# Optimization experiments

Hardware: AMD Instinct MI355X
Metric: run time of the kernel (lower is better)

Reference implementation:

```python
import jax, jax.numpy as jnp
import numpy as np

NUM_FEATURES = 256
NUM_PIDS = 5554          # must equal hardcoded FocalLoss ignore_index
NUM_CQ = 50000
N_ROIS = 2048
OIM_SCALAR = 30.0
IGNORE_INDEX = 5554
ALPHA = 1.0
GAMMA = 2.0


def _l2norm(x):
    return x / jnp.linalg.norm(x, axis=-1, keepdims=True)


def setup_inputs() -> dict:
    key = jax.random.key(0)
    k1, k2, k3, k4, k5 = jax.random.split(key, 5)
    inputs = _l2norm(jax.random.normal(k1, (N_ROIS, NUM_FEATURES), jnp.float32))
    # targets >= 1 so label = targets-1 >= 0 (the inds filter is all-True -> static shapes)
    # targets == NUM_PIDS+1 -> label == NUM_PIDS == ignore_index (unlabeled, ignored in loss)
    targets = jax.random.randint(k2, (N_ROIS,), 1, NUM_PIDS + 2, dtype=jnp.int64)
    ious = jax.random.uniform(k3, (N_ROIS,), jnp.float32)
    lut = _l2norm(jax.random.normal(k4, (NUM_PIDS, NUM_FEATURES), jnp.float32))
    cq = _l2norm(jax.random.normal(k5, (NUM_CQ, NUM_FEATURES), jnp.float32))
    return {"inputs": inputs, "lut": lut, "cq": cq, "targets": targets, "ious": ious}


def _focal_loss(logits, labels):
    # F.cross_entropy(reduction='none', ignore_index=IGNORE_INDEX) then
    # focal = alpha * (1-pt)^gamma * ce, mean over ALL samples (ignored -> 0).
    logp = jax.nn.log_softmax(logits, axis=-1)                       # [N, C]
    ce = -jnp.take_along_axis(logp, labels[:, None], axis=1)[:, 0]   # [N]
    ce = jnp.where(labels == IGNORE_INDEX, 0.0, ce)
    pt = jnp.exp(-ce)
    return jnp.mean(ALPHA * (1.0 - pt) ** GAMMA * ce)


def reference(inputs, lut, cq, targets, ious):
    # targets = cat(roi_label); label = targets - 1; inds all True by construction.
    label = targets - 1
    # LOIM forward: logits against labeled LUT and unlabeled circular queue.
    table = jnp.concatenate([lut, cq], axis=0)          # [P+Q, D]
    projected = OIM_SCALAR * (inputs @ table.T)         # [N, P+Q]
    loss_oim = _focal_loss(projected, label)
    return loss_oim, inputs, label
```

## Files before the change

### kernel.cpp

```cpp
#include <hip/hip_runtime.h>
#include <hip/hip_bf16.h>


#define NFEAT 256
#define NROIS 2048
#define NPIDS 5554
#define NCLS 55554
#define NCHUNKS 3473
#define S2F 43.280851226668906f
#define LN2F 0.6931471805599453f
#define LOFF 524289

typedef float f32x4 __attribute__((ext_vector_type(4)));
typedef short bf16x8 __attribute__((ext_vector_type(8)));

#if __has_builtin(__builtin_amdgcn_exp2f)
#define EXP2(x) __builtin_amdgcn_exp2f(x)
#else
#define EXP2(x) exp2f(x)
#endif

__device__ __forceinline__ short bfb(float x) {
    return __builtin_bit_cast(short, __float2bfloat16(x));
}

__global__ __launch_bounds__(256) void prep(const int* __restrict__ cand0,
                                            const int* __restrict__ cand1,
                                            int* __restrict__ lab,
                                            float* __restrict__ S) {
    __shared__ int smode;
    __shared__ const int* sT;
    if (threadIdx.x == 0) {
        const int* T = cand0;
        const unsigned u0 = (unsigned)cand0[0];
        const float f0 = __builtin_bit_cast(float, cand0[0]);
        const bool oki = (u0 >= 1u && u0 <= 6000u);
        const bool okf = (f0 >= 1.0f && f0 <= 6000.0f);
        if (!oki && !okf) T = cand1;
        int mode = 0;
        const unsigned tu0 = (unsigned)T[0];
        const float tf0 = __builtin_bit_cast(float, T[0]);
        if (tu0 >= 1u && tu0 <= 6000u) mode = ((T[1] | T[3] | T[5] | T[7]) == 0) ? 1 : 0;
        else if (tf0 >= 1.0f && tf0 <= 6000.0f) mode = 2;
        smode = mode; sT = T;
    }
    __syncthreads();
    const int mode = smode;
    const int* T = sT;
    for (int j = threadIdx.x; j < NROIS; j += 256) {
        int tv;
        if (mode == 1)      tv = T[2 * j];
        else if (mode == 2) tv = (int)__builtin_bit_cast(float, T[j]);
        else                tv = T[j];
        lab[j] = tv - 1;
    }
    for (int j = threadIdx.x; j < NROIS + 1; j += 256) S[j] = 0.0f;
}

__global__ __launch_bounds__(256) void cvt_table(const float* __restrict__ lut,
                                                 const float* __restrict__ cq,
                                                 unsigned short* __restrict__ tb) {
    const size_t LUTN = (size_t)NPIDS * NFEAT;
    const size_t TOT  = (size_t)NCLS * NFEAT;
    size_t i = ((size_t)blockIdx.x * 256 + threadIdx.x) * 4;
    const size_t stride = (size_t)gridDim.x * 256 * 4;
    for (; i < TOT; i += stride) {
        float4 v;
        if (i < LUTN) v = *reinterpret_cast<const float4*>(lut + i);
        else          v = *reinterpret_cast<const float4*>(cq + (i - LUTN));
        ushort4 o;
        o.x = (unsigned short)bfb(v.x); o.y = (unsigned short)bfb(v.y);
        o.z = (unsigned short)bfb(v.z); o.w = (unsigned short)bfb(v.w);
        *reinterpret_cast<ushort4*>(tb + i) = o;
    }
}

__global__ __launch_bounds__(256) void writeout(const float* __restrict__ inputs,
                                                const int* __restrict__ lab,
                                                float* __restrict__ f) {
    const int i = blockIdx.x * 256 + threadIdx.x;
    const float4 v = *reinterpret_cast<const float4*>(inputs + (size_t)i * 4);
    float* o = f + 1 + (size_t)i * 4;
    o[0] = v.x; o[1] = v.y; o[2] = v.z; o[3] = v.w;
    if (i < NROIS) f[LOFF + i] = __bfloat162float(__float2bfloat16((float)lab[i]));
}

template <bool TB>
__global__ __launch_bounds__(256, 2) void main_gemm2(const float* __restrict__ inputs,
                                                     const unsigned short* __restrict__ tb,
                                                     const float* __restrict__ lut,
                                                     const float* __restrict__ cq,
                                                     float* __restrict__ S) {
    __shared__ short ldsb[2][4096];
    const int tid = threadIdx.x;
    const int lane = tid & 63;
    const int wave = tid >> 6;
    const int cs = blockIdx.x & 63;
    const int rg = blockIdx.x >> 6;
    const int rowbase = rg * 256 + wave * 64;
    const int li = lane & 15;
    const int q = lane >> 4;
    const int xorli = 4 * (li & 7);

    bf16x8 afrag[4][8];
    #pragma unroll
    for (int s = 0; s < 4; s++) {
        const float* rp = inputs + (size_t)(rowbase + s * 16 + li) * NFEAT + q * 8;
        #pragma unroll
        for (int kc = 0; kc < 8; kc++) {
            const float4 x0 = *reinterpret_cast<const float4*>(rp + kc * 32);
            const float4 x1 = *reinterpret_cast<const float4*>(rp + kc * 32 + 4);
            bf16x8 a;
            a[0] = bfb(x0.x); a[1] = bfb(x0.y); a[2] = bfb(x0.z); a[3] = bfb(x0.w);
            a[4] = bfb(x1.x); a[5] = bfb(x1.y); a[6] = bfb(x1.z); a[7] = bfb(x1.w);
            afrag[s][kc] = a;
        }
    }

    const int s0 = tid, s1 = tid + 256;
    const int cc0 = s0 >> 5, cc1 = s1 >> 5;
    const int uo0 = ((s0 & 31) ^ (4 * (cc0 & 7))) * 8;
    const int uo1 = ((s1 & 31) ^ (4 * (cc1 & 7))) * 8;

    const int cA = (cs * NCHUNKS) >> 6;
    const int cB = ((cs + 1) * NCHUNKS) >> 6;

    float sums[4][4] = {{0.f,0.f,0.f,0.f},{0.f,0.f,0.f,0.f},
                        {0.f,0.f,0.f,0.f},{0.f,0.f,0.f,0.f}};

    {
        int n0 = cA * 16 + cc0; n0 = n0 < (NCLS - 1) ? n0 : (NCLS - 1);
        int n1 = cA * 16 + cc1; n1 = n1 < (NCLS - 1) ? n1 : (NCLS - 1);
        if (TB) {
            const bf16x8 v0 = *reinterpret_cast<const bf16x8*>(tb + (size_t)n0 * NFEAT + uo0);
            const bf16x8 v1 = *reinterpret_cast<const bf16x8*>(tb + (size_t)n1 * NFEAT + uo1);
            *reinterpret_cast<bf16x8*>(&ldsb[0][s0 * 8]) = v0;
            *reinterpret_cast<bf16x8*>(&ldsb[0][s1 * 8]) = v1;
        } else {
            const float* r0 = ((n0 < NPIDS) ? lut + (size_t)n0 * NFEAT
                                            : cq + (size_t)(n0 - NPIDS) * NFEAT) + uo0;
            const float* r1 = ((n1 < NPIDS) ? lut + (size_t)n1 * NFEAT
                                            : cq + (size_t)(n1 - NPIDS) * NFEAT) + uo1;
            const float4 a0 = *reinterpret_cast<const float4*>(r0);
            const float4 a1 = *reinterpret_cast<const float4*>(r0 + 4);
            const float4 b0 = *reinterpret_cast<const float4*>(r1);
            const float4 b1 = *reinterpret_cast<const float4*>(r1 + 4);
            bf16x8 v0, v1;
            v0[0]=bfb(a0.x); v0[1]=bfb(a0.y); v0[2]=bfb(a0.z); v0[3]=bfb(a0.w);
            v0[4]=bfb(a1.x); v0[5]=bfb(a1.y); v0[6]=bfb(a1.z); v0[7]=bfb(a1.w);
            v1[0]=bfb(b0.x); v1[1]=bfb(b0.y); v1[2]=bfb(b0.z); v1[3]=bfb(b0.w);
            v1[4]=bfb(b1.x); v1[5]=bfb(b1.y); v1[6]=bfb(b1.z); v1[7]=bfb(b1.w);
            *reinterpret_cast<bf16x8*>(&ldsb[0][s0 * 8]) = v0;
            *reinterpret_cast<bf16x8*>(&ldsb[0][s1 * 8]) = v1;
        }
    }
    __syncthreads();

    int cur = 0;
    for (int ci = cA; ci < cB; ++ci) {
        const bool pf = (ci + 1 < cB);
        bf16x8 p0, p1;
        float4 f0a, f0b, f1a, f1b;
        if (pf) {
            int n0 = (ci + 1) * 16 + cc0; n0 = n0 < (NCLS - 1) ? n0 : (NCLS - 1);
            int n1 = (ci + 1) * 16 + cc1; n1 = n1 < (NCLS - 1) ? n1 : (NCLS - 1);
            if (TB) {
                p0 = *reinterpret_cast<const bf16x8*>(tb + (size_t)n0 * NFEAT + uo0);
                p1 = *reinterpret_cast<const bf16x8*>(tb + (size_t)n1 * NFEAT + uo1);
            } else {
                const float* r0 = ((n0 < NPIDS) ? lut + (size_t)n0 * NFEAT
                                                : cq + (size_t)(n0 - NPIDS) * NFEAT) + uo0;
                const float* r1 = ((n1 < NPIDS) ? lut + (size_t)n1 * NFEAT
                                                : cq + (size_t)(n1 - NPIDS) * NFEAT) + uo1;
                f0a = *reinterpret_cast<const float4*>(r0);
                f0b = *reinterpret_cast<const float4*>(r0 + 4);
                f1a = *reinterpret_cast<const float4*>(r1);
                f1b = *reinterpret_cast<const float4*>(r1 + 4);
            }
        }
        f32x4 acc[4] = {{0.f,0.f,0.f,0.f},{0.f,0.f,0.f,0.f},
                        {0.f,0.f,0.f,0.f},{0.f,0.f,0.f,0.f}};
        #pragma unroll
        for (int kc = 0; kc < 8; kc++) {
            const int slot = li * 32 + ((q + 4 * kc) ^ xorli);
            const bf16x8 b = *reinterpret_cast<const bf16x8*>(&ldsb[cur][slot * 8]);
            acc[0] = __builtin_amdgcn_mfma_f32_16x16x32_bf16(afrag[0][kc], b, acc[0], 0, 0, 0);
            acc[1] = __builtin_amdgcn_mfma_f32_16x16x32_bf16(afrag[1][kc], b, acc[1], 0, 0, 0);
            acc[2] = __builtin_amdgcn_mfma_f32_16x16x32_bf16(afrag[2][kc], b, acc[2], 0, 0, 0);
            acc[3] = __builtin_amdgcn_mfma_f32_16x16x32_bf16(afrag[3][kc], b, acc[3], 0, 0, 0);
        }
        const float valid = ((ci * 16 + li) < NCLS) ? 1.0f : 0.0f;
        #pragma unroll
        for (int s = 0; s < 4; s++)
            #pragma unroll
            for (int r = 0; r < 4; r++)
                sums[s][r] += valid * EXP2(S2F * (acc[s][r] - 1.0f));
        if (pf) {
            if (!TB) {
                p0[0]=bfb(f0a.x); p0[1]=bfb(f0a.y); p0[2]=bfb(f0a.z); p0[3]=bfb(f0a.w);
                p0[4]=bfb(f0b.x); p0[5]=bfb(f0b.y); p0[6]=bfb(f0b.z); p0[7]=bfb(f0b.w);
                p1[0]=bfb(f1a.x); p1[1]=bfb(f1a.y); p1[2]=bfb(f1a.z); p1[3]=bfb(f1a.w);
                p1[4]=bfb(f1b.x); p1[5]=bfb(f1b.y); p1[6]=bfb(f1b.z); p1[7]=bfb(f1b.w);
            }
            *reinterpret_cast<bf16x8*>(&ldsb[cur ^ 1][s0 * 8]) = p0;
            *reinterpret_cast<bf16x8*>(&ldsb[cur ^ 1][s1 * 8]) = p1;
        }
        __syncthreads();
        cur ^= 1;
    }

    #pragma unroll
    for (int s = 0; s < 4; s++)
        #pragma unroll
        for (int r = 0; r < 4; r++) {
            float v = sums[s][r];
            v += __shfl_xor(v, 1); v += __shfl_xor(v, 2);
            v += __shfl_xor(v, 4); v += __shfl_xor(v, 8);
            sums[s][r] = v;
        }
    if (li == 0) {
        #pragma unroll
        for (int s = 0; s < 4; s++)
            #pragma unroll
            for (int r = 0; r < 4; r++)
                atomicAdd(&S[rowbase + s * 16 + q * 4 + r], sums[s][r]);
    }
}

__global__ __launch_bounds__(256) void focal_final(const float* __restrict__ inputs,
                                                   const float* __restrict__ lut,
                                                   const int* __restrict__ lab,
                                                   const float* __restrict__ S,
                                                   float* __restrict__ loss_acc) {
    const int wave = threadIdx.x >> 6;
    const int lane = threadIdx.x & 63;
    const int row = blockIdx.x * 4 + wave;
    const int label = lab[row];
    const bool valid = (label >= 0 && label < NPIDS);
    const int lr = valid ? label : 0;
    const float4 a = *reinterpret_cast<const float4*>(inputs + (size_t)row * NFEAT + lane * 4);
    const float4 b = *reinterpret_cast<const float4*>(lut + (size_t)lr * NFEAT + lane * 4);
    float v = a.x * b.x + a.y * b.y + a.z * b.z + a.w * b.w;
    #pragma unroll
    for (int m = 1; m < 64; m <<= 1) v += __shfl_xor(v, m);

    __shared__ float red[4];
    if (lane == 0) {
        float fo = 0.0f;
        if (valid) {
            const float l2 = v * S2F;
            const float lse2 = S2F + log2f(S[row]);
            float ce = fmaxf((lse2 - l2) * LN2F, 0.0f);
            const float pt = EXP2(l2 - lse2);
            const float om = 1.0f - pt;
            fo = om * om * ce;
        }
        red[wave] = fo;
    }
    __syncthreads();
    if (threadIdx.x == 0) atomicAdd(loss_acc, red[0] + red[1] + red[2] + red[3]);
}

__global__ void loss_write(const float* __restrict__ loss_acc, float* __restrict__ f) {
    if (threadIdx.x == 0 && blockIdx.x == 0) f[0] = loss_acc[0] * (1.0f / NROIS);
}

extern "C" void kernel_launch(void* const* d_in, const int* in_sizes, int n_in,
                              void* d_out, int out_size, void* d_ws, size_t ws_size,
                              hipStream_t stream) {
    const float* inputs = (const float*)d_in[0];
    const float* lut    = (const float*)d_in[1];
    const float* cq     = (const float*)d_in[2];
    const int*   cand0  = (const int*)d_in[3];
    const int*   cand1  = (const int*)((n_in > 4) ? d_in[4] : d_in[3]);
    float* f = (float*)d_out;

    const size_t TBB = (size_t)NCLS * NFEAT * 2;
    char* ws = (char*)d_ws;
    const bool useTB = ws_size >= TBB + 32768;

    unsigned short* tb = useTB ? (unsigned short*)ws : nullptr;
    float* S        = useTB ? (float*)(ws + TBB) : (float*)ws;
    float* loss_acc = S + NROIS;
    int*   lab      = (int*)(S + NROIS + 1);

    prep<<<1, 256, 0, stream>>>(cand0, cand1, lab, S);
    if (useTB) cvt_table<<<4096, 256, 0, stream>>>(lut, cq, tb);
    writeout<<<512, 256, 0, stream>>>(inputs, lab, f);
    if (useTB) main_gemm2<true><<<512, 256, 0, stream>>>(inputs, tb, lut, cq, S);
    else       main_gemm2<false><<<512, 256, 0, stream>>>(inputs, tb, lut, cq, S);
    focal_final<<<512, 256, 0, stream>>>(inputs, lut, lab, S, loss_acc);
    loss_write<<<1, 64, 0, stream>>>(loss_acc, f);
}
```

Baseline: 193.0 us.

## Fuse preprocessing kernels, triple-buffer GEMM with direct global-to-LDS loads

Merges prep, table conversion and writeout into one preprocessing kernel that also pre-converts inputs to bf16 and pads the table with zero rows. The GEMM's fast path now streams table tiles straight into LDS with global_load_lds into a three-stage ring guarded by manual waitcnt/barrier, which removes register staging and the per-chunk validity mask. The final loss write is folded into focal_final through a last-block counter. Together these cut kernel launches and load latency, at the cost of extra workspace and reliance on hand-written waitcnt ordering. Padded rows still add exp(-S2F) terms, which is only a tiny approximation.

Result: faster. 176.7 us (-8.5%).

```diff
diff --git a/kernel.cpp b/kernel.cpp
--- a/kernel.cpp
+++ b/kernel.cpp
@@ -7,12 +7,14 @@
 #define NPIDS 5554
 #define NCLS 55554
 #define NCHUNKS 3473
+#define NCLSP (NCHUNKS * 16)
 #define S2F 43.280851226668906f
 #define LN2F 0.6931471805599453f
 #define LOFF 524289
 
 typedef float f32x4 __attribute__((ext_vector_type(4)));
 typedef short bf16x8 __attribute__((ext_vector_type(8)));
+typedef unsigned short u16x8 __attribute__((ext_vector_type(8)));
 
 #if __has_builtin(__builtin_amdgcn_exp2f)
 #define EXP2(x) __builtin_amdgcn_exp2f(x)
@@ -24,74 +26,95 @@
     return __builtin_bit_cast(short, __float2bfloat16(x));
 }
 
-__global__ __launch_bounds__(256) void prep(const int* __restrict__ cand0,
-                                            const int* __restrict__ cand1,
-                                            int* __restrict__ lab,
-                                            float* __restrict__ S) {
-    __shared__ int smode;
-    __shared__ const int* sT;
-    if (threadIdx.x == 0) {
-        const int* T = cand0;
-        const unsigned u0 = (unsigned)cand0[0];
-        const float f0 = __builtin_bit_cast(float, cand0[0]);
-        const bool oki = (u0 >= 1u && u0 <= 6000u);
-        const bool okf = (f0 >= 1.0f && f0 <= 6000.0f);
-        if (!oki && !okf) T = cand1;
-        int mode = 0;
-        const unsigned tu0 = (unsigned)T[0];
-        const float tf0 = __builtin_bit_cast(float, T[0]);
-        if (tu0 >= 1u && tu0 <= 6000u) mode = ((T[1] | T[3] | T[5] | T[7]) == 0) ? 1 : 0;
-        else if (tf0 >= 1.0f && tf0 <= 6000.0f) mode = 2;
-        smode = mode; sT = T;
-    }
-    __syncthreads();
-    const int mode = smode;
-    const int* T = sT;
-    for (int j = threadIdx.x; j < NROIS; j += 256) {
-        int tv;
-        if (mode == 1)      tv = T[2 * j];
-        else if (mode == 2) tv = (int)__builtin_bit_cast(float, T[j]);
-        else                tv = T[j];
-        lab[j] = tv - 1;
-    }
-    for (int j = threadIdx.x; j < NROIS + 1; j += 256) S[j] = 0.0f;
-}
-
-__global__ __launch_bounds__(256) void cvt_table(const float* __restrict__ lut,
-                                                 const float* __restrict__ cq,
-                                                 unsigned short* __restrict__ tb) {
-    const size_t LUTN = (size_t)NPIDS * NFEAT;
-    const size_t TOT  = (size_t)NCLS * NFEAT;
-    size_t i = ((size_t)blockIdx.x * 256 + threadIdx.x) * 4;
-    const size_t stride = (size_t)gridDim.x * 256 * 4;
-    for (; i < TOT; i += stride) {
-        float4 v;
-        if (i < LUTN) v = *reinterpret_cast<const float4*>(lut + i);
-        else          v = *reinterpret_cast<const float4*>(cq + (i - LUTN));
-        ushort4 o;
-        o.x = (unsigned short)bfb(v.x); o.y = (unsigned short)bfb(v.y);
-        o.z = (unsigned short)bfb(v.z); o.w = (unsigned short)bfb(v.w);
-        *reinterpret_cast<ushort4*>(tb + i) = o;
-    }
-}
-
-__global__ __launch_bounds__(256) void writeout(const float* __restrict__ inputs,
-                                                const int* __restrict__ lab,
-                                                float* __restrict__ f) {
-    const int i = blockIdx.x * 256 + threadIdx.x;
-    const float4 v = *reinterpret_cast<const float4*>(inputs + (size_t)i * 4);
-    float* o = f + 1 + (size_t)i * 4;
-    o[0] = v.x; o[1] = v.y; o[2] = v.z; o[3] = v.w;
-    if (i < NROIS) f[LOFF + i] = __bfloat162float(__float2bfloat16((float)lab[i]));
+__device__ __forceinline__ void gll16(const void* g, void* l) {
+    __builtin_amdgcn_global_load_lds(
+        (const __attribute__((address_space(1))) void*)g,
+        (__attribute__((address_space(3))) void*)l, 16, 0, 0);
+}
+
+__global__ __launch_bounds__(256) void preprocess(
+        const float* __restrict__ inputs, const float* __restrict__ lut,
+        const float* __restrict__ cq, const int* __restrict__ cand0,
+        const int* __restrict__ cand1, unsigned short* __restrict__ tb,
+        unsigned short* __restrict__ ab, int* __restrict__ lab,
+        float* __restrict__ S, float* __restrict__ f, const int useTB) {
+    const int tid = threadIdx.x;
+    const int bx = blockIdx.x;
+
+    if (bx == 0) {
+        __shared__ int smode;
+        __shared__ const int* sT;
+        if (tid == 0) {
+            const int* T = cand0;
+            const unsigned u0 = (unsigned)cand0[0];
+            const float f0 = __builtin_bit_cast(float, cand0[0]);
+            const bool oki = (u0 >= 1u && u0 <= 6000u);
+            const bool okf = (f0 >= 1.0f && f0 <= 6000.0f);
+            if (!oki && !okf) T = cand1;
+            int mode = 0;
+            const unsigned tu0 = (unsigned)T[0];
+            const float tf0 = __builtin_bit_cast(float, T[0]);
+            if (tu0 >= 1u && tu0 <= 6000u) mode = ((T[1] | T[3] | T[5] | T[7]) == 0) ? 1 : 0;
+            else if (tf0 >= 1.0f && tf0 <= 6000.0f) mode = 2;
+            smode = mode; sT = T;
+        }
+        __syncthreads();
+        const int mode = smode;
+        const int* T = sT;
+        for (int j = tid; j < NROIS; j += 256) {
+            int tv;
+            if (mode == 1)      tv = T[2 * j];
+            else if (mode == 2) tv = (int)__builtin_bit_cast(float, T[j]);
+            else                tv = T[j];
+            const int lv = tv - 1;
+            lab[j] = lv;
+            f[LOFF + j] = __bfloat162float(__float2bfloat16((float)lv));
+        }
+        for (int j = tid; j < NROIS + 8; j += 256) S[j] = 0.0f;
+    }
+
+    if (bx < 512) {
+        const int i = bx * 256 + tid;
+        const float4 v = *reinterpret_cast<const float4*>(inputs + (size_t)i * 4);
+        float* o = f + 1 + (size_t)i * 4;
+        o[0] = v.x; o[1] = v.y; o[2] = v.z; o[3] = v.w;
+        if (useTB) {
+            ushort4 u;
+            u.x = (unsigned short)bfb(v.x); u.y = (unsigned short)bfb(v.y);
+            u.z = (unsigned short)bfb(v.z); u.w = (unsigned short)bfb(v.w);
+            *reinterpret_cast<ushort4*>(ab + (size_t)i * 4) = u;
+        }
+    }
+
+    if (useTB) {
+        const size_t LUTN = (size_t)NPIDS * NFEAT;
+        const size_t TOT  = (size_t)NCLS * NFEAT;
+        const size_t TOTP = (size_t)NCLSP * NFEAT;
+        const size_t stride = (size_t)gridDim.x * 256 * 8;
+        for (size_t e = ((size_t)bx * 256 + tid) * 8; e < TOTP; e += stride) {
+            u16x8 o = {0, 0, 0, 0, 0, 0, 0, 0};
+            if (e < TOT) {
+                const float* sp = (e < LUTN) ? (lut + e) : (cq + (e - LUTN));
+                const float4 a = *reinterpret_cast<const float4*>(sp);
+                const float4 b = *reinterpret_cast<const float4*>(sp + 4);
+                o[0] = (unsigned short)bfb(a.x); o[1] = (unsigned short)bfb(a.y);
+                o[2] = (unsigned short)bfb(a.z); o[3] = (unsigned short)bfb(a.w);
+                o[4] = (unsigned short)bfb(b.x); o[5] = (unsigned short)bfb(b.y);
+                o[6] = (unsigned short)bfb(b.z); o[7] = (unsigned short)bfb(b.w);
+            }
+            *reinterpret_cast<u16x8*>(tb + e) = o;
+        }
+    }
 }
 
 template <bool TB>
-__global__ __launch_bounds__(256, 2) void main_gemm2(const float* __restrict__ inputs,
+__global__ __launch_bounds__(256, 2) void main_gemm3(const float* __restrict__ inputs,
                                                      const unsigned short* __restrict__ tb,
+                                                     const unsigned short* __restrict__ ab,
                                                      const float* __restrict__ lut,
                                                      const float* __restrict__ cq,
                                                      float* __restrict__ S) {
-    __shared__ short ldsb[2][4096];
+    __shared__ short ldsb[3][4096];
     const int tid = threadIdx.x;
     const int lane = tid & 63;
     const int wave = tid >> 6;
@@ -103,17 +126,27 @@
     const int xorli = 4 * (li & 7);
 
     bf16x8 afrag[4][8];
-    #pragma unroll
-    for (int s = 0; s < 4; s++) {
-        const float* rp = inputs + (size_t)(rowbase + s * 16 + li) * NFEAT + q * 8;
+    if constexpr (TB) {
         #pragma unroll
-        for (int kc = 0; kc < 8; kc++) {
-            const float4 x0 = *reinterpret_cast<const float4*>(rp + kc * 32);
-            const float4 x1 = *reinterpret_cast<const float4*>(rp + kc * 32 + 4);
-            bf16x8 a;
-            a[0] = bfb(x0.x); a[1] = bfb(x0.y); a[2] = bfb(x0.z); a[3] = bfb(x0.w);
-            a[4] = bfb(x1.x); a[5] = bfb(x1.y); a[6] = bfb(x1.z); a[7] = bfb(x1.w);
-            afrag[s][kc] = a;
+        for (int s = 0; s < 4; s++) {
+            const unsigned short* rp = ab + (size_t)(rowbase + s * 16 + li) * NFEAT + q * 8;
+            #pragma unroll
+            for (int kc = 0; kc < 8; kc++)
+                afrag[s][kc] = *reinterpret_cast<const bf16x8*>(rp + kc * 32);
+        }
+    } else {
+        #pragma unroll
+        for (int s = 0; s < 4; s++) {
+            const float* rp = inputs + (size_t)(rowbase + s * 16 + li) * NFEAT + q * 8;
+            #pragma unroll
+            for (int kc = 0; kc < 8; kc++) {
+                const float4 x0 = *reinterpret_cast<const float4*>(rp + kc * 32);
+                const float4 x1 = *reinterpret_cast<const float4*>(rp + kc * 32 + 4);
+                bf16x8 a;
+                a[0] = bfb(x0.x); a[1] = bfb(x0.y); a[2] = bfb(x0.z); a[3] = bfb(x0.w);
+                a[4] = bfb(x1.x); a[5] = bfb(x1.y); a[6] = bfb(x1.z); a[7] = bfb(x1.w);
+                afrag[s][kc] = a;
+            }
         }
     }
 
@@ -124,19 +157,58 @@
 
     const int cA = (cs * NCHUNKS) >> 6;
     const int cB = ((cs + 1) * NCHUNKS) >> 6;
+    const int NB = cB - cA;
 
     float sums[4][4] = {{0.f,0.f,0.f,0.f},{0.f,0.f,0.f,0.f},
                         {0.f,0.f,0.f,0.f},{0.f,0.f,0.f,0.f}};
-
-    {
-        int n0 = cA * 16 + cc0; n0 = n0 < (NCLS - 1) ? n0 : (NCLS - 1);
-        int n1 = cA * 16 + cc1; n1 = n1 < (NCLS - 1) ? n1 : (NCLS - 1);
-        if (TB) {
-            const bf16x8 v0 = *reinterpret_cast<const bf16x8*>(tb + (size_t)n0 * NFEAT + uo0);
-            const bf16x8 v1 = *reinterpret_cast<const bf16x8*>(tb + (size_t)n1 * NFEAT + uo1);
-            *reinterpret_cast<bf16x8*>(&ldsb[0][s0 * 8]) = v0;
-            *reinterpret_cast<bf16x8*>(&ldsb[0][s1 * 8]) = v1;
-        } else {
+    char* const lbase = (char*)&ldsb[0][0];
+
+    if constexpr (TB) {
+        const int ld0 = wave * 1024;
+        const int ld1 = 4096 + wave * 1024;
+        const unsigned short* p0 = tb + (size_t)(cA * 16 + cc0) * NFEAT + uo0;
+        const unsigned short* p1 = tb + (size_t)(cA * 16 + cc1) * NFEAT + uo1;
+        int ob0 = 0, ob1 = 8192, ob2 = 16384;
+
+        gll16(p0, lbase + ob0 + ld0);
+        gll16(p1, lbase + ob0 + ld1);
+        p0 += 16 * NFEAT; p1 += 16 * NFEAT;
+        if (NB > 1) {
+            gll16(p0, lbase + ob1 + ld0);
+            gll16(p1, lbase + ob1 + ld1);
+            p0 += 16 * NFEAT; p1 += 16 * NFEAT;
+        }
+
+        for (int i = 0; i < NB; ++i) {
+            if (i + 1 < NB) asm volatile("s_waitcnt vmcnt(2)\n\ts_barrier" ::: "memory");
+            else            asm volatile("s_waitcnt vmcnt(0)\n\ts_barrier" ::: "memory");
+            if (i + 2 < NB) {
+                gll16(p0, lbase + ob2 + ld0);
+                gll16(p1, lbase + ob2 + ld1);
+                p0 += 16 * NFEAT; p1 += 16 * NFEAT;
+            }
+            f32x4 acc[4] = {{0.f,0.f,0.f,0.f},{0.f,0.f,0.f,0.f},
+                            {0.f,0.f,0.f,0.f},{0.f,0.f,0.f,0.f}};
+            #pragma unroll
+            for (int kc = 0; kc < 8; kc++) {
+                const int slot = li * 32 + ((q + 4 * kc) ^ xorli);
+                const bf16x8 b = *reinterpret_cast<const bf16x8*>(lbase + ob0 + slot * 16);
+                acc[0] = __builtin_amdgcn_mfma_f32_16x16x32_bf16(afrag[0][kc], b, acc[0], 0, 0, 0);
+                acc[1] = __builtin_amdgcn_mfma_f32_16x16x32_bf16(afrag[1][kc], b, acc[1], 0, 0, 0);
+                acc[2] = __builtin_amdgcn_mfma_f32_16x16x32_bf16(afrag[2][kc], b, acc[2], 0, 0, 0);
+                acc[3] = __builtin_amdgcn_mfma_f32_16x16x32_bf16(afrag[3][kc], b, acc[3], 0, 0, 0);
+            }
+            #pragma unroll
+            for (int s = 0; s < 4; s++)
+                #pragma unroll
+                for (int r = 0; r < 4; r++)
+                    sums[s][r] += EXP2(S2F * acc[s][r] - S2F);
+            const int t = ob0; ob0 = ob1; ob1 = ob2; ob2 = t;
+        }
+    } else {
+        {
+            int n0 = cA * 16 + cc0; n0 = n0 < (NCLS - 1) ? n0 : (NCLS - 1);
+            int n1 = cA * 16 + cc1; n1 = n1 < (NCLS - 1) ? n1 : (NCLS - 1);
             const float* r0 = ((n0 < NPIDS) ? lut + (size_t)n0 * NFEAT
                                             : cq + (size_t)(n0 - NPIDS) * NFEAT) + uo0;
             const float* r1 = ((n1 < NPIDS) ? lut + (size_t)n1 * NFEAT
@@ -153,21 +225,14 @@
             *reinterpret_cast<bf16x8*>(&ldsb[0][s0 * 8]) = v0;
             *reinterpret_cast<bf16x8*>(&ldsb[0][s1 * 8]) = v1;
         }
-    }
-    __syncthreads();
-
-    int cur = 0;
-    for (int ci = cA; ci < cB; ++ci) {
-        const bool pf = (ci + 1 < cB);
-        bf16x8 p0, p1;
-        float4 f0a, f0b, f1a, f1b;
-        if (pf) {
-            int n0 = (ci + 1) * 16 + cc0; n0 = n0 < (NCLS - 1) ? n0 : (NCLS - 1);
-            int n1 = (ci + 1) * 16 + cc1; n1 = n1 < (NCLS - 1) ? n1 : (NCLS - 1);
-            if (TB) {
-                p0 = *reinterpret_cast<const bf16x8*>(tb + (size_t)n0 * NFEAT + uo0);
-                p1 = *reinterpret_cast<const bf16x8*>(tb + (size_t)n1 * NFEAT + uo1);
-            } else {
+        __syncthreads();
+        int cur = 0;
+        for (int ci = cA; ci < cB; ++ci) {
+            const bool pf = (ci + 1 < cB);
+            float4 f0a, f0b, f1a, f1b;
+            if (pf) {
+                int n0 = (ci + 1) * 16 + cc0; n0 = n0 < (NCLS - 1) ? n0 : (NCLS - 1);
+                int n1 = (ci + 1) * 16 + cc1; n1 = n1 < (NCLS - 1) ? n1 : (NCLS - 1);
                 const float* r0 = ((n0 < NPIDS) ? lut + (size_t)n0 * NFEAT
                                                 : cq + (size_t)(n0 - NPIDS) * NFEAT) + uo0;
                 const float* r1 = ((n1 < NPIDS) ? lut + (size_t)n1 * NFEAT
@@ -177,36 +242,35 @@
                 f1a = *reinterpret_cast<const float4*>(r1);
                 f1b = *reinterpret_cast<const float4*>(r1 + 4);
             }
-        }
-        f32x4 acc[4] = {{0.f,0.f,0.f,0.f},{0.f,0.f,0.f,0.f},
-                        {0.f,0.f,0.f,0.f},{0.f,0.f,0.f,0.f}};
-        #pragma unroll
-        for (int kc = 0; kc < 8; kc++) {
-            const int slot = li * 32 + ((q + 4 * kc) ^ xorli);
-            const bf16x8 b = *reinterpret_cast<const bf16x8*>(&ldsb[cur][slot * 8]);
-            acc[0] = __builtin_amdgcn_mfma_f32_16x16x32_bf16(afrag[0][kc], b, acc[0], 0, 0, 0);
-            acc[1] = __builtin_amdgcn_mfma_f32_16x16x32_bf16(afrag[1][kc], b, acc[1], 0, 0, 0);
-            acc[2] = __builtin_amdgcn_mfma_f32_16x16x32_bf16(afrag[2][kc], b, acc[2], 0, 0, 0);
-            acc[3] = __builtin_amdgcn_mfma_f32_16x16x32_bf16(afrag[3][kc], b, acc[3], 0, 0, 0);
-        }
-        const float valid = ((ci * 16 + li) < NCLS) ? 1.0f : 0.0f;
-        #pragma unroll
-        for (int s = 0; s < 4; s++)
-            #pragma unroll
-            for (int r = 0; r < 4; r++)
-                sums[s][r] += valid * EXP2(S2F * (acc[s][r] - 1.0f));
-        if (pf) {
-            if (!TB) {
+            f32x4 acc[4] = {{0.f,0.f,0.f,0.f},{0.f,0.f,0.f,0.f},
+                            {0.f,0.f,0.f,0.f},{0.f,0.f,0.f,0.f}};
+            #pragma unroll
+            for (int kc = 0; kc < 8; kc++) {
+                const int slot = li * 32 + ((q + 4 * kc) ^ xorli);
+                const bf16x8 b = *reinterpret_cast<const bf16x8*>(&ldsb[cur][slot * 8]);
+                acc[0] = __builtin_amdgcn_mfma_f32_16x16x32_bf16(afrag[0][kc], b, acc[0], 0, 0, 0);
+                acc[1] = __builtin_amdgcn_mfma_f32_16x16x32_bf16(afrag[1][kc], b, acc[1], 0, 0, 0);
+                acc[2] = __builtin_amdgcn_mfma_f32_16x16x32_bf16(afrag[2][kc], b, acc[2], 0, 0, 0);
+                acc[3] = __builtin_amdgcn_mfma_f32_16x16x32_bf16(afrag[3][kc], b, acc[3], 0, 0, 0);
+            }
+            const float valid = ((ci * 16 + li) < NCLS) ? 1.0f : 0.0f;
+            #pragma unroll
+            for (int s = 0; s < 4; s++)
+                #pragma unroll
+                for (int r = 0; r < 4; r++)
+                    sums[s][r] += valid * EXP2(S2F * (acc[s][r] - 1.0f));
+            if (pf) {
+                bf16x8 p0, p1;
                 p0[0]=bfb(f0a.x); p0[1]=bfb(f0a.y); p0[2]=bfb(f0a.z); p0[3]=bfb(f0a.w);
                 p0[4]=bfb(f0b.x); p0[5]=bfb(f0b.y); p0[6]=bfb(f0b.z); p0[7]=bfb(f0b.w);
                 p1[0]=bfb(f1a.x); p1[1]=bfb(f1a.y); p1[2]=bfb(f1a.z); p1[3]=bfb(f1a.w);
                 p1[4]=bfb(f1b.x); p1[5]=bfb(f1b.y); p1[6]=bfb(f1b.z); p1[7]=bfb(f1b.w);
-            }
-            *reinterpret_cast<bf16x8*>(&ldsb[cur ^ 1][s0 * 8]) = p0;
-            *reinterpret_cast<bf16x8*>(&ldsb[cur ^ 1][s1 * 8]) = p1;
-        }
-        __syncthreads();
-        cur ^= 1;
+                *reinterpret_cast<bf16x8*>(&ldsb[cur ^ 1][s0 * 8]) = p0;
+                *reinterpret_cast<bf16x8*>(&ldsb[cur ^ 1][s1 * 8]) = p1;
+            }
+            __syncthreads();
+            cur ^= 1;
+        }
     }
 
     #pragma unroll
@@ -231,7 +295,9 @@
                                                    const float* __restrict__ lut,
                                                    const int* __restrict__ lab,
                                                    const float* __restrict__ S,
-                                                   float* __restrict__ loss_acc) {
+                                                   float* __restrict__ loss_acc,
+                                                   unsigned int* __restrict__ cnt,
+                                                   float* __restrict__ f) {
     const int wave = threadIdx.x >> 6;
     const int lane = threadIdx.x & 63;
     const int row = blockIdx.x * 4 + wave;
@@ -258,11 +324,15 @@
         red[wave] = fo;
     }
     __syncthreads();
-    if (threadIdx.x == 0) atomicAdd(loss_acc, red[0] + red[1] + red[2] + red[3]);
-}
-
-__global__ void loss_write(const float* __restrict__ loss_acc, float* __restrict__ f) {
-    if (threadIdx.x == 0 && blockIdx.x == 0) f[0] = loss_acc[0] * (1.0f / NROIS);
+    if (threadIdx.x == 0) {
+        atomicAdd(loss_acc, red[0] + red[1] + red[2] + red[3]);
+        __threadfence();
+        const unsigned done = atomicAdd(cnt, 1u) + 1u;
+        if (done == gridDim.x) {
+            const float tot = atomicAdd(loss_acc, 0.0f);
+            f[0] = tot * (1.0f / NROIS);
+        }
+    }
 }
 
 extern "C" void kernel_launch(void* const* d_in, const int* in_sizes, int n_in,
@@ -275,20 +345,21 @@
     const int*   cand1  = (const int*)((n_in > 4) ? d_in[4] : d_in[3]);
     float* f = (float*)d_out;
 
-    const size_t TBB = (size_t)NCLS * NFEAT * 2;
+    const size_t TBB = (size_t)NCLSP * NFEAT * 2;
+    const size_t ABB = (size_t)NROIS * NFEAT * 2;
     char* ws = (char*)d_ws;
-    const bool useTB = ws_size >= TBB + 32768;
+    const bool useTB = ws_size >= TBB + ABB + 32768;
 
     unsigned short* tb = useTB ? (unsigned short*)ws : nullptr;
-    float* S        = useTB ? (float*)(ws + TBB) : (float*)ws;
-    float* loss_acc = S + NROIS;
-    int*   lab      = (int*)(S + NROIS + 1);
-
-    prep<<<1, 256, 0, stream>>>(cand0, cand1, lab, S);
-    if (useTB) cvt_table<<<4096, 256, 0, stream>>>(lut, cq, tb);
-    writeout<<<512, 256, 0, stream>>>(inputs, lab, f);
-    if (useTB) main_gemm2<true><<<512, 256, 0, stream>>>(inputs, tb, lut, cq, S);
-    else       main_gemm2<false><<<512, 256, 0, stream>>>(inputs, tb, lut, cq, S);
-    focal_final<<<512, 256, 0, stream>>>(inputs, lut, lab, S, loss_acc);
-    loss_write<<<1, 64, 0, stream>>>(loss_acc, f);
-}
+    unsigned short* ab = useTB ? (unsigned short*)(ws + TBB) : nullptr;
+    float* S = useTB ? (float*)(ws + TBB + ABB) : (float*)ws;
+    float* loss_acc    = S + NROIS;
+    unsigned int* cnt  = (unsigned int*)(S + NROIS + 1);
+    int* lab           = (int*)(S + NROIS + 8);
+
+    preprocess<<<useTB ? 4096 : 512, 256, 0, stream>>>(inputs, lut, cq, cand0, cand1,
+                                                       tb, ab, lab, S, f, useTB ? 1 : 0);
+    if (useTB) main_gemm3<true><<<512, 256, 0, stream>>>(inputs, tb, ab, lut, cq, S);
+    else       main_gemm3<false><<<512, 256, 0, stream>>>(inputs, tb, ab, lut, cq, S);
+    focal_final<<<512, 256, 0, stream>>>(inputs, lut, lab, S, loss_acc, cnt, f);
+}
```
